# Performance work log

Measured on AMD Instinct MI355X. Metric: run time of the kernel, lower is better.

## Reference

```python
import jax, jax.numpy as jnp
import numpy as np

N_NODES = 50000
N_EDGES = 800000
D_IN = 256
D_HID = 256
N_CLASSES = 40


def gcn_conv(x, W, b, src, dst, deg_inv_sqrt, n):
    # PyG GCNConv: linear transform first, then normalized scatter-add aggregation.
    x = x @ W                                   # [N, d_out]
    norm = deg_inv_sqrt[src] * deg_inv_sqrt[dst]  # [E+N] sym norm with self-loops
    msgs = x[src] * norm[:, None]               # gather source features
    out = jax.ops.segment_sum(msgs, dst, num_segments=n)
    return out + b


def setup_inputs() -> dict:
    key = jax.random.key(0)
    ks = jax.random.split(key, 6)
    x = jax.random.normal(ks[0], (N_NODES, D_IN), dtype=jnp.float32)
    edge_index = jax.random.randint(ks[1], (2, N_EDGES), 0, N_NODES, dtype=jnp.int64)
    s_in = 1.0 / np.sqrt(D_IN)
    s_h = 1.0 / np.sqrt(D_HID)
    W0 = jax.random.normal(ks[2], (D_IN, D_HID), dtype=jnp.float32) * s_in
    b0 = jnp.zeros((D_HID,), dtype=jnp.float32)
    W1 = jax.random.normal(ks[3], (D_HID, D_HID), dtype=jnp.float32) * s_h
    b1 = jnp.zeros((D_HID,), dtype=jnp.float32)
    W2 = jax.random.normal(ks[4], (D_HID, N_CLASSES), dtype=jnp.float32) * s_h
    b2 = jnp.zeros((N_CLASSES,), dtype=jnp.float32)
    return {"x": x, "edge_index": edge_index, "W0": W0, "b0": b0,
            "W1": W1, "b1": b1, "W2": W2, "b2": b2}


def reference(x, edge_index, W0, b0, W1, b1, W2, b2):
    n = x.shape[0]
    loops = jnp.arange(n, dtype=edge_index.dtype)
    src = jnp.concatenate([edge_index[0], loops])
    dst = jnp.concatenate([edge_index[1], loops])
    # degree (with self-loops) on destination nodes; deg >= 1 so rsqrt is safe
    deg = jax.ops.segment_sum(jnp.ones_like(dst, dtype=x.dtype), dst, num_segments=n)
    deg_inv_sqrt = jax.lax.rsqrt(deg)

    h = gcn_conv(x, W0, b0, src, dst, deg_inv_sqrt, n)
    h = jax.nn.relu(h)  # dropout is identity in eval mode
    h = gcn_conv(h, W1, b1, src, dst, deg_inv_sqrt, n)
    h = jax.nn.relu(h)
    h = gcn_conv(h, W2, b2, src, dst, deg_inv_sqrt, n)
    return jax.nn.log_softmax(h, axis=1)
```

## Files before the change

### kernel.cpp

```cpp
#include <hip/hip_runtime.h>
#include <hip/hip_bf16.h>
#include <cstdint>
#include <cstddef>


typedef unsigned char u8;
typedef unsigned short u16;
typedef unsigned int u32;
typedef __attribute__((ext_vector_type(8))) short bf16x8;
typedef __attribute__((ext_vector_type(4))) float f32x4;
typedef __attribute__((ext_vector_type(2))) float f32x2;

__device__ inline u16 f2bf(float f) {
  __hip_bfloat16 h = __float2bfloat16(f);
  return __builtin_bit_cast(u16, h);
}
__device__ inline u32 pk2bf(float lo, float hi) {
  return ((u32)f2bf(hi) << 16) | (u32)f2bf(lo);
}
__device__ inline u32 pk4fp8(float a, float b, float c, float d) {
  u32 w = __builtin_amdgcn_cvt_pk_fp8_f32(a, b, 0, false);
  w = __builtin_amdgcn_cvt_pk_fp8_f32(c, d, w, true);
  return w;
}
__device__ inline void up4fp8(u32 w, float* a) {
  f32x2 lo = __builtin_amdgcn_cvt_pk_f32_fp8(w, false);
  f32x2 hi = __builtin_amdgcn_cvt_pk_f32_fp8(w, true);
  a[0] += lo[0]; a[1] += lo[1]; a[2] += hi[0]; a[3] += hi[1];
}

__device__ inline void gl_lds16(const u16* g, u16* ldsbase) {
  __builtin_amdgcn_global_load_lds(
      (const __attribute__((address_space(1))) u32*)g,
      (__attribute__((address_space(3))) u32*)ldsbase, 16, 0, 0);
}

__global__ void k_prepcvtcount(const float* __restrict__ W0,
                               const float* __restrict__ W1,
                               const float* __restrict__ W2,
                               u16* __restrict__ Wt0, u16* __restrict__ Wt1,
                               u16* __restrict__ Wt2, int* __restrict__ bflag,
                               u8* __restrict__ zu8, u8* __restrict__ z40,
                               const float* __restrict__ x, u16* __restrict__ xb,
                               int total8,
                               const int* __restrict__ dst, int* __restrict__ cnt,
                               int* __restrict__ rank, int E,
                               int PB, int VB, int n) {
  const int bid = blockIdx.x;
  if (bid < PB) {
    const int t = bid * 256 + threadIdx.x;
    if (t < 65536) {
      const int k = t >> 8, c = t & 255;
      Wt0[c * 256 + k] = f2bf(W0[t]);
      Wt1[c * 256 + k] = f2bf(W1[t]);
    } else if (t < 65536 + 16384) {
      const int t2 = t - 65536;
      const int k = t2 >> 6, nn = t2 & 63;
      const float v = (nn < 40) ? W2[k * 40 + nn] : 0.f;
      Wt2[nn * 256 + k] = f2bf(v);
    } else {
      const int u = t - (65536 + 16384);
      if (u < 64) bflag[u] = 0;
      if (u < 256) zu8[u] = 0;
      if (u < 40) z40[u] = 0;
    }
    return;
  }
  if (bid < PB + VB) {
    const int i = (bid - PB) * 256 + threadIdx.x;
    if (i < total8) {
      const float4 lo = ((const float4*)x)[2 * i];
      const float4 hi = ((const float4*)x)[2 * i + 1];
      uint4 w;
      w.x = pk2bf(lo.x, lo.y); w.y = pk2bf(lo.z, lo.w);
      w.z = pk2bf(hi.x, hi.y); w.w = pk2bf(hi.z, hi.w);
      ((uint4*)xb)[i] = w;
    }
    return;
  }
  const int e = (bid - PB - VB) * 256 + threadIdx.x;
  if (e < E) rank[e] = atomicAdd(&cnt[dst[e]], 1);
}

__global__ __launch_bounds__(1024) void k_scan(const int* __restrict__ cnt,
                                               int* __restrict__ rs,
                                               float* __restrict__ dis,
                                               int* __restrict__ bval,
                                               int* __restrict__ bpre,
                                               int* __restrict__ bflag, int n) {
  __shared__ int wsum[16];
  __shared__ int sbase;
  const int b = blockIdx.x;
  const int tid = threadIdx.x;
  const int lane = tid & 63, wid = tid >> 6;
  const int i = b * 1024 + tid;
  const int v = (i < n) ? cnt[i] : 0;
  int x = v;
#pragma unroll
  for (int off = 1; off < 64; off <<= 1) {
    int y = __shfl_up(x, off, 64);
    if (lane >= off) x += y;
  }
  if (lane == 63) wsum[wid] = x;
  __syncthreads();
  if (wid == 0) {
    int w = (lane < 16) ? wsum[lane] : 0;
#pragma unroll
    for (int off = 1; off < 16; off <<= 1) {
      int y = __shfl_up(w, off, 64);
      if (lane >= off) w += y;
    }
    if (lane < 16) wsum[lane] = w;
  }
  __syncthreads();
  const int total = wsum[15];
  const int excl = (wid > 0 ? wsum[wid - 1] : 0) + (x - v);

  if (tid == 0) {
    if (b == 0) {
      atomicExch(&bpre[0], total);
      __threadfence();
      atomicExch(&bflag[0], 2);
      sbase = 0;
    } else {
      atomicExch(&bval[b], total);
      __threadfence();
      atomicExch(&bflag[b], 1);
      int run = 0, j = b - 1;
      while (true) {
        int f;
        while ((f = atomicAdd(&bflag[j], 0)) == 0) {}
        if (f == 2) { run += atomicAdd(&bpre[j], 0); break; }
        run += atomicAdd(&bval[j], 0);
        --j;
      }
      atomicExch(&bpre[b], run + total);
      __threadfence();
      atomicExch(&bflag[b], 2);
      sbase = run;
    }
  }
  __syncthreads();
  const int base = sbase;
  if (i < n) {
    rs[i] = base + excl;
    dis[i] = rsqrtf((float)(1 + v));
  }
  if (b == (int)gridDim.x - 1 && tid == 0) rs[n] = base + total;
}

__device__ inline void gemm256_body(const u16* __restrict__ A,
                                    const u16* __restrict__ Wt,
                                    const float* __restrict__ dis,
                                    u8* __restrict__ C, int M,
                                    int bx, int by, u16* As, u16* Bs) {
  const int tid = threadIdx.x;
  const int wid = tid >> 6, lane = tid & 63;
  const int wave_m = wid & 1, wave_n = wid >> 1;
  const int m0 = bx * 64, n0 = by * 128;
  const int quad = lane >> 4, col = lane & 15;

  const int srl = lane >> 3;
  const int sseg = lane & 7;

  const int ra = wave_m * 32 + col;
  const int rb = wave_n * 64 + col;

  f32x4 acc[2][4];
#pragma unroll
  for (int i = 0; i < 2; ++i)
#pragma unroll
    for (int j = 0; j < 4; ++j) acc[i][j] = (f32x4){0.f, 0.f, 0.f, 0.f};

  for (int k0 = 0; k0 < 256; k0 += 64) {
#pragma unroll
    for (int blk = 0; blk < 2; ++blk) {
      const int R = wid * 16 + blk * 8;
      const int r = R + srl;
      const int q = (sseg - r) & 7;
      if (m0 + r < M)
        gl_lds16(A + (size_t)(m0 + r) * 256 + k0 + q * 8, &As[R * 64]);
    }
#pragma unroll
    for (int blk = 0; blk < 4; ++blk) {
      const int R = wid * 32 + blk * 8;
      const int r = R + srl;
      const int q = (sseg - r) & 7;
      gl_lds16(Wt + (size_t)(n0 + r) * 256 + k0 + q * 8, &Bs[R * 64]);
    }
    __syncthreads();

#pragma unroll
    for (int kk = 0; kk < 2; ++kk) {
      bf16x8 af[2], bf[4];
#pragma unroll
      for (int i = 0; i < 2; ++i) {
        const int r = ra + i * 16;
        af[i] = *(const bf16x8*)&As[r * 64 + ((quad + kk * 4 + r) & 7) * 8];
      }
#pragma unroll
      for (int j = 0; j < 4; ++j) {
        const int r = rb + j * 16;
        bf[j] = *(const bf16x8*)&Bs[r * 64 + ((quad + kk * 4 + r) & 7) * 8];
      }
#pragma unroll
      for (int i = 0; i < 2; ++i)
#pragma unroll
        for (int j = 0; j < 4; ++j)
          acc[i][j] = __builtin_amdgcn_mfma_f32_16x16x32_bf16(bf[j], af[i], acc[i][j], 0, 0, 0);
    }
    __syncthreads();
  }

#pragma unroll
  for (int i = 0; i < 2; ++i) {
    const int m = m0 + wave_m * 32 + i * 16 + col;
    if (m < M) {
      const float dd = dis[m];
#pragma unroll
      for (int j = 0; j < 4; ++j) {
        const int n = n0 + wave_n * 64 + j * 16 + quad * 4;
        const u32 w = pk4fp8(acc[i][j][0] * dd, acc[i][j][1] * dd,
                             acc[i][j][2] * dd, acc[i][j][3] * dd);
        *(u32*)(C + (size_t)m * 256 + n) = w;
      }
    }
  }
}

__global__ __launch_bounds__(256) void k_gemmfill(
    const u16* __restrict__ xb, const u16* __restrict__ Wt0,
    const float* __restrict__ dis, u8* __restrict__ C, int M,
    const int* __restrict__ src, const int* __restrict__ dst,
    const int* __restrict__ rank, const int* __restrict__ rs,
    int* __restrict__ csr, int E, int GB) {
  __shared__ u16 As[64 * 64];
  __shared__ u16 Bs[128 * 64];
  if ((int)blockIdx.x >= GB) {
    const int e = (blockIdx.x - GB) * 256 + threadIdx.x;
    if (e < E) csr[rs[dst[e]] + rank[e]] = src[e];
    return;
  }
  gemm256_body(xb, Wt0, dis, C, M, blockIdx.x >> 1, blockIdx.x & 1, As, Bs);
}

__global__ __launch_bounds__(256) void k_gemm256(const u16* __restrict__ A,
                                                 const u16* __restrict__ Wt,
                                                 const float* __restrict__ dis,
                                                 u8* __restrict__ C, int M) {
  __shared__ u16 As[64 * 64];
  __shared__ u16 Bs[128 * 64];
  gemm256_body(A, Wt, dis, C, M, blockIdx.x, blockIdx.y, As, Bs);
}

__global__ __launch_bounds__(256) void k_agg256(const u8* __restrict__ u,
                                                const int* __restrict__ rs,
                                                const int* __restrict__ csr,
                                                const float* __restrict__ dis,
                                                const float* __restrict__ b,
                                                u16* __restrict__ out, int n) {
  const int wid = threadIdx.x >> 6, lane = threadIdx.x & 63;
  const int d = blockIdx.x * 4 + wid;
  if (d >= n) return;
  const int q = lane >> 4, sl = lane & 15;
  const int cb = sl * 16;
  float a[16] = {0.f, 0.f, 0.f, 0.f, 0.f, 0.f, 0.f, 0.f,
                 0.f, 0.f, 0.f, 0.f, 0.f, 0.f, 0.f, 0.f};
  {
    const int sidx = q ? n : d;
    const uint4 v = *(const uint4*)(u + (size_t)sidx * 256 + cb);
    up4fp8(v.x, a); up4fp8(v.y, a + 4); up4fp8(v.z, a + 8); up4fp8(v.w, a + 12);
  }
  const int p1 = rs[d + 1];
  for (int p = rs[d]; p < p1; p += 16) {
    int idx[4];
#pragma unroll
    for (int i = 0; i < 4; ++i) {
      const int e = p + 4 * i + q;
      idx[i] = (e < p1) ? csr[e] : n;
    }
    uint4 v[4];
#pragma unroll
    for (int i = 0; i < 4; ++i)
      v[i] = *(const uint4*)(u + (size_t)idx[i] * 256 + cb);
#pragma unroll
    for (int i = 0; i < 4; ++i) {
      up4fp8(v[i].x, a); up4fp8(v[i].y, a + 4);
      up4fp8(v[i].z, a + 8); up4fp8(v[i].w, a + 12);
    }
  }
#pragma unroll
  for (int j = 0; j < 16; ++j) {
    a[j] += __shfl_xor(a[j], 16, 64);
    a[j] += __shfl_xor(a[j], 32, 64);
  }
  if (q == 0) {
    const float dd = dis[d];
    uint4 o0, o1;
    const float4 b0 = *(const float4*)(b + cb);
    const float4 b1 = *(const float4*)(b + cb + 4);
    const float4 b2 = *(const float4*)(b + cb + 8);
    const float4 b3 = *(const float4*)(b + cb + 12);
    o0.x = pk2bf(fmaxf(dd * a[0] + b0.x, 0.f), fmaxf(dd * a[1] + b0.y, 0.f));
    o0.y = pk2bf(fmaxf(dd * a[2] + b0.z, 0.f), fmaxf(dd * a[3] + b0.w, 0.f));
    o0.z = pk2bf(fmaxf(dd * a[4] + b1.x, 0.f), fmaxf(dd * a[5] + b1.y, 0.f));
    o0.w = pk2bf(fmaxf(dd * a[6] + b1.z, 0.f), fmaxf(dd * a[7] + b1.w, 0.f));
    o1.x = pk2bf(fmaxf(dd * a[8] + b2.x, 0.f), fmaxf(dd * a[9] + b2.y, 0.f));
    o1.y = pk2bf(fmaxf(dd * a[10] + b2.z, 0.f), fmaxf(dd * a[11] + b2.w, 0.f));
    o1.z = pk2bf(fmaxf(dd * a[12] + b3.x, 0.f), fmaxf(dd * a[13] + b3.y, 0.f));
    o1.w = pk2bf(fmaxf(dd * a[14] + b3.z, 0.f), fmaxf(dd * a[15] + b3.w, 0.f));
    *(uint4*)(out + (size_t)d * 256 + cb) = o0;
    *(uint4*)(out + (size_t)d * 256 + cb + 8) = o1;
  }
}

__global__ __launch_bounds__(256) void k_gemm40(const u16* __restrict__ A,
                                                const u16* __restrict__ Wt2,
                                                const float* __restrict__ dis,
                                                u8* __restrict__ C, int M) {
  const int wv = threadIdx.x >> 6, lane = threadIdx.x & 63;
  const int quad = lane >> 4, col = lane & 15;
  const int m0 = blockIdx.x * 128 + wv * 32;
  f32x4 acc[2][3];
#pragma unroll
  for (int i = 0; i < 2; ++i)
#pragma unroll
    for (int j = 0; j < 3; ++j) acc[i][j] = (f32x4){0.f, 0.f, 0.f, 0.f};
  for (int k0 = 0; k0 < 256; k0 += 32) {
    bf16x8 af[2], bf[3];
#pragma unroll
    for (int i = 0; i < 2; ++i) {
      int row = m0 + i * 16 + col;
      row = (row < M) ? row : (M - 1);
      af[i] = *(const bf16x8*)(A + (size_t)row * 256 + k0 + quad * 8);
    }
#pragma unroll
    for (int j = 0; j < 3; ++j)
      bf[j] = *(const bf16x8*)(Wt2 + (size_t)(j * 16 + col) * 256 + k0 + quad * 8);
#pragma unroll
    for (int i = 0; i < 2; ++i)
#pragma unroll
      for (int j = 0; j < 3; ++j)
        acc[i][j] = __builtin_amdgcn_mfma_f32_16x16x32_bf16(bf[j], af[i], acc[i][j], 0, 0, 0);
  }
#pragma unroll
  for (int i = 0; i < 2; ++i) {
    const int m = m0 + i * 16 + col;
    if (m < M) {
      const float dd = dis[m];
#pragma unroll
      for (int j = 0; j < 3; ++j) {
        const int nn = j * 16 + quad * 4;
        if (nn < 40) {
          const u32 w = pk4fp8(acc[i][j][0] * dd, acc[i][j][1] * dd,
                               acc[i][j][2] * dd, acc[i][j][3] * dd);
          *(u32*)(C + (size_t)m * 40 + nn) = w;
        }
      }
    }
  }
}

__global__ __launch_bounds__(256) void k_agg40(const u8* __restrict__ u,
                                               const int* __restrict__ rs,
                                               const int* __restrict__ csr,
                                               const float* __restrict__ dis,
                                               const float* __restrict__ b,
                                               float* __restrict__ out, int n) {
  const int wid = threadIdx.x >> 6, lane = threadIdx.x & 63;
  const int d = blockIdx.x * 4 + wid;
  if (d >= n) return;
  const int slot = lane / 10;
  const int sl = lane % 10;
  const bool act = slot < 6;
  float a[4] = {0.f, 0.f, 0.f, 0.f};
  if (slot == 0) {
    const u32 v = *(const u32*)(u + (size_t)d * 40 + sl * 4);
    up4fp8(v, a);
  }
  const int p1 = rs[d + 1];
  for (int p = rs[d]; p < p1; p += 24) {
    int idx[4];
#pragma unroll
    for (int i = 0; i < 4; ++i) {
      const int e = p + 6 * i + slot;
      idx[i] = (act && e < p1) ? csr[e] : n;
    }
    u32 v[4];
#pragma unroll
    for (int i = 0; i < 4; ++i)
      v[i] = *(const u32*)(u + (size_t)idx[i] * 40 + sl * 4);
#pragma unroll
    for (int i = 0; i < 4; ++i) up4fp8(v[i], a);
  }
#pragma unroll
  for (int k = 0; k < 4; ++k) {
    const float t = __shfl(a[k], lane + 30, 64);
    a[k] += t;
  }
#pragma unroll
  for (int k = 0; k < 4; ++k) {
    const float t1 = __shfl(a[k], lane + 10, 64);
    const float t2 = __shfl(a[k], lane + 20, 64);
    a[k] += t1 + t2;
  }
  float l[4];
  float mx = -INFINITY;
  const bool head = lane < 10;
  if (head) {
    const float dd = dis[d];
#pragma unroll
    for (int k = 0; k < 4; ++k) {
      l[k] = dd * a[k] + b[lane * 4 + k];
      mx = fmaxf(mx, l[k]);
    }
  }
#pragma unroll
  for (int off = 8; off; off >>= 1) mx = fmaxf(mx, __shfl_xor(mx, off, 64));
  float sm = 0.f;
  if (head) {
#pragma unroll
    for (int k = 0; k < 4; ++k) sm += expf(l[k] - mx);
  }
#pragma unroll
  for (int off = 8; off; off >>= 1) sm += __shfl_xor(sm, off, 64);
  if (head) {
    const float ls = mx + logf(sm);
    float4 o = make_float4(l[0] - ls, l[1] - ls, l[2] - ls, l[3] - ls);
    *(float4*)(out + (size_t)d * 40 + lane * 4) = o;
  }
}

extern "C" void kernel_launch(void* const* d_in, const int* in_sizes, int n_in,
                              void* d_out, int out_size, void* d_ws, size_t ws_size,
                              hipStream_t stream) {
  const float* x  = (const float*)d_in[0];
  const int*   ei = (const int*)d_in[1];
  const float* W0 = (const float*)d_in[2];
  const float* b0 = (const float*)d_in[3];
  const float* W1 = (const float*)d_in[4];
  const float* b1 = (const float*)d_in[5];
  const float* W2 = (const float*)d_in[6];
  const float* b2 = (const float*)d_in[7];
  float* out = (float*)d_out;

  const int N = in_sizes[0] / 256;
  const int E = in_sizes[1] / 2;
  const int* src = ei;
  const int* dst = ei + E;

  char* p = (char*)d_ws;
  auto carve = [&](size_t bytes) {
    char* q = p;
    p += (bytes + 255) & ~(size_t)255;
    return q;
  };
  u16*   xb    = (u16*)carve((size_t)N * 256 * 2);
  u8*    uf8   = (u8*)carve((size_t)(N + 1) * 256);
  u16*   h     = (u16*)carve((size_t)N * 256 * 2);
  u8*    u40   = (u8*)carve((size_t)(N + 1) * 40);
  u16*   Wt0   = (u16*)carve(256 * 256 * 2);
  u16*   Wt1   = (u16*)carve(256 * 256 * 2);
  u16*   Wt2   = (u16*)carve(64 * 256 * 2);
  float* dis   = (float*)carve((size_t)N * 4);
  int*   cnt   = (int*)carve((size_t)N * 4);
  int*   rs    = (int*)carve((size_t)(N + 1) * 4);
  int*   rank  = (int*)carve((size_t)E * 4);
  int*   csr   = (int*)carve((size_t)(E + 32) * 4);
  int*   bval  = (int*)carve(64 * 4);
  int*   bpre  = (int*)carve(64 * 4);
  int*   bflag = (int*)carve(64 * 4);

  const int PB = (65536 + 16384 + 256 + 255) / 256;
  const int total8 = N * 256 / 8;
  const int VB = (total8 + 255) / 256;
  const int CB = (E + 255) / 256;
  const int GB = ((N + 63) / 64) * 2;
  const int nb = (N + 1023) / 1024;
  const int agrid = (N + 3) / 4;

  hipMemsetAsync(cnt, 0, (size_t)N * 4, stream);

  k_prepcvtcount<<<PB + VB + CB, 256, 0, stream>>>(
      W0, W1, W2, Wt0, Wt1, Wt2, bflag,
      uf8 + (size_t)N * 256, u40 + (size_t)N * 40,
      x, xb, total8, dst, cnt, rank, E, PB, VB, N);
  k_scan<<<nb, 1024, 0, stream>>>(cnt, rs, dis, bval, bpre, bflag, N);
  k_gemmfill<<<GB + CB, 256, 0, stream>>>(xb, Wt0, dis, uf8, N,
                                          src, dst, rank, rs, csr, E, GB);
  k_agg256<<<agrid, 256, 0, stream>>>(uf8, rs, csr, dis, b0, h, N);
  k_gemm256<<<dim3((N + 63) / 64, 2), 256, 0, stream>>>(h, Wt1, dis, uf8, N);
  k_agg256<<<agrid, 256, 0, stream>>>(uf8, rs, csr, dis, b1, h, N);
  k_gemm40<<<(N + 127) / 128, 256, 0, stream>>>(h, Wt2, dis, u40, N);
  k_agg40<<<agrid, 256, 0, stream>>>(u40, rs, csr, dis, b2, out, N);
}
```

Measured before the change: 306.5 us.

## Build CSR with cursor atomics instead of per-edge rank array; predicate gathers

The count pass no longer stores each edge's atomic return value as a rank. The fill pass instead atomically bumps a per-node cursor, initialised by the scan, to place each source index. This removes the E-sized rank array write and read at the cost of a second round of atomics, and it makes neighbour order within a CSR row nondeterministic. The fill blocks now come before the GEMM blocks in the fused launch. The aggregation loops skip out-of-range slots with a predicate rather than loading a zeroed dummy row, so the sentinel rows and their zeroing are removed.

Result: slower. 384.5 us (+25.5%).

```diff
diff --git a/kernel.cpp b/kernel.cpp
--- a/kernel.cpp
+++ b/kernel.cpp
@@ -40,12 +40,10 @@
                                const float* __restrict__ W2,
                                u16* __restrict__ Wt0, u16* __restrict__ Wt1,
                                u16* __restrict__ Wt2, int* __restrict__ bflag,
-                               u8* __restrict__ zu8, u8* __restrict__ z40,
                                const float* __restrict__ x, u16* __restrict__ xb,
                                int total8,
                                const int* __restrict__ dst, int* __restrict__ cnt,
-                               int* __restrict__ rank, int E,
-                               int PB, int VB, int n) {
+                               int E, int PB, int VB, int n) {
   const int bid = blockIdx.x;
   if (bid < PB) {
     const int t = bid * 256 + threadIdx.x;
@@ -61,8 +59,6 @@
     } else {
       const int u = t - (65536 + 16384);
       if (u < 64) bflag[u] = 0;
-      if (u < 256) zu8[u] = 0;
-      if (u < 40) z40[u] = 0;
     }
     return;
   }
@@ -79,11 +75,12 @@
     return;
   }
   const int e = (bid - PB - VB) * 256 + threadIdx.x;
-  if (e < E) rank[e] = atomicAdd(&cnt[dst[e]], 1);
+  if (e < E) atomicAdd(&cnt[dst[e]], 1);
 }
 
 __global__ __launch_bounds__(1024) void k_scan(const int* __restrict__ cnt,
                                                int* __restrict__ rs,
+                                               int* __restrict__ cur,
                                                float* __restrict__ dis,
                                                int* __restrict__ bval,
                                                int* __restrict__ bpre,
@@ -143,7 +140,9 @@
   __syncthreads();
   const int base = sbase;
   if (i < n) {
-    rs[i] = base + excl;
+    const int r = base + excl;
+    rs[i] = r;
+    cur[i] = r;
     dis[i] = rsqrtf((float)(1 + v));
   }
   if (b == (int)gridDim.x - 1 && tid == 0) rs[n] = base + total;
@@ -228,20 +227,23 @@
   }
 }
 
-__global__ __launch_bounds__(256) void k_gemmfill(
+__global__ __launch_bounds__(256) void k_fillgemm(
     const u16* __restrict__ xb, const u16* __restrict__ Wt0,
     const float* __restrict__ dis, u8* __restrict__ C, int M,
     const int* __restrict__ src, const int* __restrict__ dst,
-    const int* __restrict__ rank, const int* __restrict__ rs,
-    int* __restrict__ csr, int E, int GB) {
+    int* __restrict__ cur, int* __restrict__ csr, int E, int FB) {
   __shared__ u16 As[64 * 64];
   __shared__ u16 Bs[128 * 64];
-  if ((int)blockIdx.x >= GB) {
-    const int e = (blockIdx.x - GB) * 256 + threadIdx.x;
-    if (e < E) csr[rs[dst[e]] + rank[e]] = src[e];
+  if ((int)blockIdx.x < FB) {
+    const int e = blockIdx.x * 256 + threadIdx.x;
+    if (e < E) {
+      const int pos = atomicAdd(&cur[dst[e]], 1);
+      csr[pos] = src[e];
+    }
     return;
   }
-  gemm256_body(xb, Wt0, dis, C, M, blockIdx.x >> 1, blockIdx.x & 1, As, Bs);
+  const int bb = blockIdx.x - FB;
+  gemm256_body(xb, Wt0, dis, C, M, bb >> 1, bb & 1, As, Bs);
 }
 
 __global__ __launch_bounds__(256) void k_gemm256(const u16* __restrict__ A,
@@ -266,23 +268,22 @@
   const int cb = sl * 16;
   float a[16] = {0.f, 0.f, 0.f, 0.f, 0.f, 0.f, 0.f, 0.f,
                  0.f, 0.f, 0.f, 0.f, 0.f, 0.f, 0.f, 0.f};
-  {
-    const int sidx = q ? n : d;
-    const uint4 v = *(const uint4*)(u + (size_t)sidx * 256 + cb);
+  if (q == 0) {
+    const uint4 v = *(const uint4*)(u + (size_t)d * 256 + cb);
     up4fp8(v.x, a); up4fp8(v.y, a + 4); up4fp8(v.z, a + 8); up4fp8(v.w, a + 12);
   }
   const int p1 = rs[d + 1];
   for (int p = rs[d]; p < p1; p += 16) {
-    int idx[4];
+    uint4 v[4];
 #pragma unroll
     for (int i = 0; i < 4; ++i) {
       const int e = p + 4 * i + q;
-      idx[i] = (e < p1) ? csr[e] : n;
-    }
-    uint4 v[4];
-#pragma unroll
-    for (int i = 0; i < 4; ++i)
-      v[i] = *(const uint4*)(u + (size_t)idx[i] * 256 + cb);
+      v[i] = make_uint4(0u, 0u, 0u, 0u);
+      if (e < p1) {
+        const int idx = csr[e];
+        v[i] = *(const uint4*)(u + (size_t)idx * 256 + cb);
+      }
+    }
 #pragma unroll
     for (int i = 0; i < 4; ++i) {
       up4fp8(v[i].x, a); up4fp8(v[i].y, a + 4);
@@ -380,16 +381,16 @@
   }
   const int p1 = rs[d + 1];
   for (int p = rs[d]; p < p1; p += 24) {
-    int idx[4];
+    u32 v[4];
 #pragma unroll
     for (int i = 0; i < 4; ++i) {
       const int e = p + 6 * i + slot;
-      idx[i] = (act && e < p1) ? csr[e] : n;
-    }
-    u32 v[4];
-#pragma unroll
-    for (int i = 0; i < 4; ++i)
-      v[i] = *(const u32*)(u + (size_t)idx[i] * 40 + sl * 4);
+      v[i] = 0u;
+      if (act && e < p1) {
+        const int idx = csr[e];
+        v[i] = *(const u32*)(u + (size_t)idx * 40 + sl * 4);
+      }
+    }
 #pragma unroll
     for (int i = 0; i < 4; ++i) up4fp8(v[i], a);
   }
@@ -456,22 +457,22 @@
     return q;
   };
   u16*   xb    = (u16*)carve((size_t)N * 256 * 2);
-  u8*    uf8   = (u8*)carve((size_t)(N + 1) * 256);
+  u8*    uf8   = (u8*)carve((size_t)N * 256);
   u16*   h     = (u16*)carve((size_t)N * 256 * 2);
-  u8*    u40   = (u8*)carve((size_t)(N + 1) * 40);
+  u8*    u40   = (u8*)carve((size_t)N * 40);
   u16*   Wt0   = (u16*)carve(256 * 256 * 2);
   u16*   Wt1   = (u16*)carve(256 * 256 * 2);
   u16*   Wt2   = (u16*)carve(64 * 256 * 2);
   float* dis   = (float*)carve((size_t)N * 4);
   int*   cnt   = (int*)carve((size_t)N * 4);
   int*   rs    = (int*)carve((size_t)(N + 1) * 4);
-  int*   rank  = (int*)carve((size_t)E * 4);
+  int*   cur   = (int*)carve((size_t)N * 4);
   int*   csr   = (int*)carve((size_t)(E + 32) * 4);
   int*   bval  = (int*)carve(64 * 4);
   int*   bpre  = (int*)carve(64 * 4);
   int*   bflag = (int*)carve(64 * 4);
 
-  const int PB = (65536 + 16384 + 256 + 255) / 256;
+  const int PB = (65536 + 16384 + 64 + 255) / 256;
   const int total8 = N * 256 / 8;
   const int VB = (total8 + 255) / 256;
   const int CB = (E + 255) / 256;
@@ -483,11 +484,10 @@
 
   k_prepcvtcount<<<PB + VB + CB, 256, 0, stream>>>(
       W0, W1, W2, Wt0, Wt1, Wt2, bflag,
-      uf8 + (size_t)N * 256, u40 + (size_t)N * 40,
-      x, xb, total8, dst, cnt, rank, E, PB, VB, N);
-  k_scan<<<nb, 1024, 0, stream>>>(cnt, rs, dis, bval, bpre, bflag, N);
-  k_gemmfill<<<GB + CB, 256, 0, stream>>>(xb, Wt0, dis, uf8, N,
-                                          src, dst, rank, rs, csr, E, GB);
+      x, xb, total8, dst, cnt, E, PB, VB, N);
+  k_scan<<<nb, 1024, 0, stream>>>(cnt, rs, cur, dis, bval, bpre, bflag, N);
+  k_fillgemm<<<CB + GB, 256, 0, stream>>>(xb, Wt0, dis, uf8, N,
+                                          src, dst, cur, csr, E, CB);
   k_agg256<<<agrid, 256, 0, stream>>>(uf8, rs, csr, dis, b0, h, N);
   k_gemm256<<<dim3((N + 63) / 64, 2), 256, 0, stream>>>(h, Wt1, dis, uf8, N);
   k_agg256<<<agrid, 256, 0, stream>>>(uf8, rs, csr, dis, b1, h, N);
```
